# Optimization experiments

Measured on AMD Instinct MI355X. Metric: run time of the kernel, lower is better.

The kernel has to match this reference:

```python
import jax, jax.numpy as jnp
import numpy as np

B, SEQ, DIMS, HEAD, LAYER = 1, 8192, 1024, 16, 4
HD = DIMS // HEAD  # 64
MEL_MAX = 2595.0 * np.log10(1.0 + 4000.0 / 200.0)  # 2595*log10(21)


def _ln(x, g, b, eps=1e-5):
    m = x.mean(-1, keepdims=True)
    v = ((x - m) ** 2).mean(-1, keepdims=True)
    return (x - m) * jax.lax.rsqrt(v + eps) * g + b


def _freq_vec():
    # mask=None branch of _compute_freqs with x=None: 200*scale/1000
    scale = 10.0 ** (jnp.linspace(0.0, MEL_MAX, HD // 2) / 2595.0) - 1.0
    return 200.0 * scale / 1000.0


def _rope(x, mag):
    # x: [b,h,c,hd]; mag: [b,c] = original input mean over feature dim
    c = x.shape[2]
    t = jnp.arange(c, dtype=x.dtype)
    ang = t[:, None] * _freq_vec()[None, :]          # [c, hd/2]
    cosA, sinA = jnp.cos(ang), jnp.sin(ang)
    m = mag[:, None, :, None]                        # [b,1,c,1] (valid: b==1)
    xr, xi = x[..., 0::2], x[..., 1::2]              # complex pairs (x[2i], x[2i+1])
    outr = m * (xr * cosA - xi * sinA)
    outi = m * (xr * sinA + xi * cosA)
    return jnp.stack([outr, outi], axis=-1).reshape(x.shape)


def setup_inputs() -> dict:
    key = jax.random.key(0)
    ks = jax.random.split(key, 4)
    s = 0.02
    return {
        "x": jax.random.normal(ks[0], (B, SEQ, DIMS), jnp.float32),
        "qn_g": jnp.ones((DIMS,), jnp.float32),
        "qn_b": jnp.zeros((DIMS,), jnp.float32),
        "Wq": jax.random.normal(ks[1], (DIMS, DIMS), jnp.float32) * s,
        "bq": jnp.zeros((DIMS,), jnp.float32),
        "kvn_g": jnp.ones((DIMS,), jnp.float32),
        "kvn_b": jnp.zeros((DIMS,), jnp.float32),
        "Wkv": jax.random.normal(ks[2], (DIMS, 2 * DIMS), jnp.float32) * s,
        "bkv": jnp.zeros((2 * DIMS,), jnp.float32),
        "Wout": jax.random.normal(ks[3], (DIMS, DIMS), jnp.float32) * s,
        "bout": jnp.zeros((DIMS,), jnp.float32),
        "ln_g": jnp.ones((HD,), jnp.float32),
        "ln_b": jnp.zeros((HD,), jnp.float32),
        "skip": 0,
    }


def reference(x, qn_g, qn_b, Wq, bq, kvn_g, kvn_b, Wkv, bkv, Wout, bout, ln_g, ln_b, skip):
    b, c, d = x.shape
    # q branch: prenorm -> linear -> [b,h,c,hd]
    q = (_ln(x, qn_g, qn_b) @ Wq + bq).reshape(b, c, HEAD, HD).transpose(0, 2, 1, 3)
    # kv branch: prenorm -> linear -> split (kv, h, d) -> [2,b,h,c,hd]
    kv = (_ln(x, kvn_g, kvn_b) @ Wkv + bkv).reshape(b, c, 2, HEAD, HD).transpose(2, 0, 3, 1, 4)
    k, v = kv[0], kv[1]
    # rotary with magnitude = x.mean(-1) (xa=x passed for both q and k)
    mag = x.mean(-1)  # [b,c]
    q = _rope(q, mag)
    k = _rope(k, mag)
    # strided sparse kv: skip-int path, pattern=None
    stride = max(1, LAYER - int(skip))
    ks_ = k[:, :, ::stride, :]
    vs_ = v[:, :, ::stride, :]
    # per-head LayerNorm on q and strided k, then SDPA (non-causal, mask=None)
    qn = _ln(q, ln_g, ln_b)
    kn = _ln(ks_, ln_g, ln_b)
    scores = jnp.einsum('bhqd,bhkd->bhqk', qn, kn) / np.sqrt(HD).astype(np.float32)
    a = jnp.einsum('bhqk,bhkd->bhqd', jax.nn.softmax(scores, axis=-1), vs_)
    return a.transpose(0, 2, 1, 3).reshape(b, c, d) @ Wout + bout
```

## Files before the change

### kernel.cpp

```cpp
#include <hip/hip_runtime.h>
#include <hip/hip_bf16.h>
#include <math.h>

#define SEQ 8192
#define DIMS 1024
#define NH 16
#define HD 64

typedef _Float16 h16;
typedef __attribute__((ext_vector_type(8))) _Float16 f16x8;
typedef __attribute__((ext_vector_type(4))) _Float16 h16x4;
typedef __attribute__((ext_vector_type(4))) float f32x4;

#if defined(__has_builtin)
#if __has_builtin(__builtin_amdgcn_global_load_lds)
#define USE_GLOAD 1
#endif
#endif
#ifndef USE_GLOAD
#define USE_GLOAD 0
#endif

__device__ __forceinline__ void gload16(h16* lds, const h16* g){
#if USE_GLOAD
  __builtin_amdgcn_global_load_lds((const __attribute__((address_space(1))) void*)g,
                                   (__attribute__((address_space(3))) void*)lds, 16, 0, 0);
#endif
}

__global__ void k_ln_stats(const float* __restrict__ x, h16* __restrict__ xhat,
                           float* __restrict__ mag){
  const int row = blockIdx.x, t = threadIdx.x;
  float4 v = ((const float4*)(x + (size_t)row*DIMS))[t];
  float s = v.x+v.y+v.z+v.w;
  float s2 = v.x*v.x+v.y*v.y+v.z*v.z+v.w*v.w;
  #pragma unroll
  for(int m=1;m<64;m<<=1){ s += __shfl_xor(s,m,64); s2 += __shfl_xor(s2,m,64); }
  __shared__ float ls[4], ls2[4];
  const int wid = t>>6;
  if((t&63)==0){ ls[wid]=s; ls2[wid]=s2; }
  __syncthreads();
  s  = ls[0]+ls[1]+ls[2]+ls[3];
  s2 = ls2[0]+ls2[1]+ls2[2]+ls2[3];
  const float mean = s*(1.f/DIMS);
  const float var  = s2*(1.f/DIMS) - mean*mean;
  const float rstd = rsqrtf(var + 1e-5f);
  if(t==0) mag[row] = mean;
  h16x4 o;
  o[0] = (h16)((v.x-mean)*rstd); o[1] = (h16)((v.y-mean)*rstd);
  o[2] = (h16)((v.z-mean)*rstd); o[3] = (h16)((v.w-mean)*rstd);
  ((h16x4*)(xhat + (size_t)row*DIMS))[t] = o;
}

__global__ void k_freq(double* __restrict__ fr){
  const int d = threadIdx.x;
  if(d < 32) fr[d] = 0.2 * (pow(21.0, (double)d / 31.0) - 1.0);
}

__global__ void k_sincos(const double* __restrict__ fr, float2* __restrict__ tab){
  const int id = blockIdx.x*256 + threadIdx.x;
  const int t = id >> 5, d = id & 31;
  const double ang = (double)t * fr[d];
  const double k = rint(ang * 0.15915494309189535);
  const float red = (float)(ang - k * 6.283185307179586);
  float s, c;
  __sincosf(red, &s, &c);
  tab[id] = make_float2(c, s);
}

__global__ void k_fold_part(const float* __restrict__ W, const float* __restrict__ bln,
                            float* __restrict__ part, const int C){
  const int j = blockIdx.x*256 + threadIdx.x;
  const int ib = blockIdx.y;
  if(j >= C) return;
  float acc = 0.f;
  const int i0 = ib*64;
  #pragma unroll 4
  for(int i=i0;i<i0+64;i++) acc += bln[i]*W[(size_t)i*C + j];
  part[(size_t)ib*C + j] = acc;
}
__global__ void k_fold_sum(const float* __restrict__ part, const float* __restrict__ b0,
                           float* __restrict__ bias_out, const int C){
  const int j = blockIdx.x*256 + threadIdx.x;
  if(j >= C) return;
  float acc = b0[j];
  #pragma unroll
  for(int ib=0; ib<16; ib++) acc += part[(size_t)ib*C + j];
  bias_out[j] = acc;
}

__global__ void k_prep_w(const float* __restrict__ W, const float* __restrict__ g,
                         h16* __restrict__ Wt, const int R, const int C){
  __shared__ float tile[64][65];
  const int c0 = blockIdx.x*64, r0 = blockIdx.y*64;
  const int t = threadIdx.x;
  const int cl = t & 63, rl0 = t >> 6;
  #pragma unroll
  for(int i=0;i<16;i++){
    const int r = rl0 + i*4;
    const float w = W[(size_t)(r0+r)*C + c0 + cl];
    const float gg = g ? g[r0+r] : 1.f;
    tile[r][cl] = w*gg;
  }
  __syncthreads();
  const int jl = t >> 2, ic = (t & 3)*16;
  h16* dst = Wt + (size_t)(c0+jl)*R + r0 + ic;
  #pragma unroll
  for(int i=0;i<16;i+=4){
    h16x4 o;
    o[0] = (h16)tile[ic+i+0][jl];
    o[1] = (h16)tile[ic+i+1][jl];
    o[2] = (h16)tile[ic+i+2][jl];
    o[3] = (h16)tile[ic+i+3][jl];
    *(h16x4*)(dst + i) = o;
  }
}

template<int MODE>
__global__ __launch_bounds__(256) void k_gemm(
    const h16* __restrict__ A, const h16* __restrict__ Bt,
    const float* __restrict__ bias, float* __restrict__ Cf,
    h16* __restrict__ OutB, h16* __restrict__ vT,
    const float* __restrict__ mag, const float2* __restrict__ tab,
    const float* __restrict__ lg, const float* __restrict__ lb,
    const int N, const int* __restrict__ skip_p){
  int M = SEQ, pitchA = DIMS, st = 1;
  if(MODE==2){
    st = max(1, 4 - skip_p[0]);
    M = (SEQ + st - 1)/st;
    pitchA = st*DIMS;
  }
  const int m0 = blockIdx.y*128, n0 = blockIdx.x*128;
  if(m0 >= M) return;
  __shared__ h16 smem[(MODE==2) ? 128*136 : 8192];
  h16* As = smem;
  h16* Bs = smem + 4096;
  const int t = threadIdx.x;
  const int w = t>>6, l = t&63, l4 = l>>4, l16 = l&15;
  const int wm = w>>1, wn = w&1;
  f32x4 acc[4][4];
  #pragma unroll
  for(int i=0;i<4;i++)
    #pragma unroll
    for(int j=0;j<4;j++)
      #pragma unroll
      for(int r=0;r<4;r++) acc[i][j][r] = 0.f;
  for(int k0=0;k0<1024;k0+=32){
    __syncthreads();
    #pragma unroll
    for(int c=t;c<512;c+=256){
      const int row = c>>2, kp = (c&3)*8;
      int ar = m0+row; if(ar > M-1) ar = M-1;
#if USE_GLOAD
      gload16(&As[row*32+kp], A + (size_t)ar*pitchA + k0 + kp);
      gload16(&Bs[row*32+kp], Bt + (size_t)(n0+row)*1024 + k0 + kp);
#else
      *(f16x8*)(&As[row*32+kp]) = *(const f16x8*)(A + (size_t)ar*pitchA + k0 + kp);
      *(f16x8*)(&Bs[row*32+kp]) = *(const f16x8*)(Bt + (size_t)(n0+row)*1024 + k0 + kp);
#endif
    }
    __syncthreads();
    f16x8 af[4], bfr[4];
    #pragma unroll
    for(int i=0;i<4;i++){
      af[i]  = *(const f16x8*)(&As[(wm*64 + i*16 + l16)*32 + l4*8]);
      bfr[i] = *(const f16x8*)(&Bs[(wn*64 + i*16 + l16)*32 + l4*8]);
    }
    #pragma unroll
    for(int i=0;i<4;i++)
      #pragma unroll
      for(int j=0;j<4;j++)
        acc[i][j] = __builtin_amdgcn_mfma_f32_16x16x32_f16(af[i], bfr[j], acc[i][j], 0,0,0);
  }

  if(MODE==0){
    #pragma unroll
    for(int i=0;i<4;i++){
      const int rb = m0 + wm*64 + i*16 + l4*4;
      #pragma unroll
      for(int j=0;j<4;j++){
        const int col = n0 + wn*64 + j*16 + l16;
        const float bb = bias[col];
        #pragma unroll
        for(int r=0;r<4;r++)
          Cf[(size_t)(rb+r)*N + col] = acc[i][j][r] + bb;
      }
    }
    return;
  }

  float biasv[4];
  #pragma unroll
  for(int j=0;j<4;j++) biasv[j] = bias[n0 + wn*64 + j*16 + l16];

  const bool vpath = (MODE==2) && (n0 >= 1024);
  if(!vpath){
    float gv[4], bv[4];
    #pragma unroll
    for(int j=0;j<4;j++){ gv[j] = lg[j*16+l16]; bv[j] = lb[j*16+l16]; }
    const int h = (n0>>6) + wn;
    const float scl = (MODE==1) ? 0.125f*1.44269504f : 1.0f;
    const float sgn = (l16&1) ? 1.f : -1.f;
    #pragma unroll
    for(int i=0;i<4;i++){
      #pragma unroll
      for(int r=0;r<4;r++){
        int row = m0 + wm*64 + i*16 + l4*4 + r;
        const int rowc = (row < M) ? row : (M-1);
        const int tpos = (MODE==2) ? rowc*st : rowc;
        const float mg = mag[tpos];
        float v[4], pr[4], o4[4];
        #pragma unroll
        for(int j=0;j<4;j++) v[j] = acc[i][j][r] + biasv[j];
        #pragma unroll
        for(int j=0;j<4;j++) pr[j] = __shfl_xor(v[j], 1);
        float s1 = 0.f, s2 = 0.f;
        #pragma unroll
        for(int j=0;j<4;j++){
          const float2 cs = tab[(size_t)tpos*32 + j*8 + (l16>>1)];
          const float e = mg * (v[j]*cs.x + sgn*pr[j]*cs.y);
          o4[j] = e; s1 += e; s2 += e*e;
        }
        #pragma unroll
        for(int mm=1;mm<16;mm<<=1){ s1 += __shfl_xor(s1,mm,64); s2 += __shfl_xor(s2,mm,64); }
        const float mean = s1*(1.f/HD);
        const float var  = s2*(1.f/HD) - mean*mean;
        const float rstd = rsqrtf(var + 1e-5f);
        if(row < M){
          h16* dst = OutB + ((size_t)h*SEQ + row)*HD;
          #pragma unroll
          for(int j=0;j<4;j++)
            dst[j*16 + l16] = (h16)(((o4[j]-mean)*rstd*gv[j] + bv[j])*scl);
        }
      }
    }
  } else {
    __syncthreads();
    #pragma unroll
    for(int i=0;i<4;i++)
      #pragma unroll
      for(int j=0;j<4;j++)
        #pragma unroll
        for(int r=0;r<4;r++){
          const int key = wm*64 + i*16 + l4*4 + r;
          smem[(wn*64 + j*16 + l16)*136 + key] = (h16)(acc[i][j][r] + biasv[j]);
        }
    __syncthreads();
    const int rowT = t>>1, dh = rowT & 63, hloc = rowT>>6;
    const int hglob = ((n0-1024)>>6) + hloc;
    const h16* src = &smem[rowT*136 + (t&1)*64];
    h16* dstv = vT + ((size_t)hglob*HD + dh)*SEQ + m0 + (t&1)*64;
    #pragma unroll
    for(int c=0;c<64;c+=4)
      *(h16x4*)(dstv+c) = *(const h16x4*)(src+c);
  }
}

__global__ void k_pad_vt(h16* __restrict__ vT, const int* __restrict__ skip_p){
  const int st = max(1, 4 - skip_p[0]);
  const int n_kv = (SEQ + st - 1)/st;
  const int kb = ((n_kv + 63)/64)*64;
  const int pad = min(kb, SEQ) - n_kv;
  if(pad <= 0) return;
  const int total = NH*HD*pad;
  for(int i = threadIdx.x; i < total; i += 256){
    const int key = n_kv + (i % pad);
    const int hd = i / pad;
    vT[(size_t)hd*SEQ + key] = (h16)0.f;
  }
}

__launch_bounds__(256)
__global__ void k_attn(const h16* __restrict__ qn, const h16* __restrict__ kn,
                       const h16* __restrict__ vT, h16* __restrict__ aout,
                       const int* __restrict__ skip_p){
  const int st = max(1, 4 - skip_p[0]);
  const int n_kv = (SEQ + st - 1)/st;
  const int h = blockIdx.x, q0 = blockIdx.y*128;
  const int w = threadIdx.x >> 6, l = threadIdx.x & 63;
  const int l4 = l >> 4, l16 = l & 15;
  __shared__ __align__(16) h16 Kl[2][64*64];
  __shared__ __align__(16) h16 Vl[2][64*64];
  __shared__ __align__(16) h16 Pl[4][16*64];
  const h16* Qh = qn + (size_t)h*SEQ*HD;
  const h16* Kh = kn + (size_t)h*SEQ*HD;
  const h16* Vh = vT + (size_t)h*HD*SEQ;
  const int srow = l >> 3;
  const int scol = ((l & 7) << 4) ^ (srow << 4);
  const int swz  = (l16 & 7) << 4;

  f16x8 onesv;
  #pragma unroll
  for(int i=0;i<8;i++) onesv[i] = (h16)1.f;

  f16x8 qf[2][2];
  #pragma unroll
  for(int mi=0;mi<2;mi++)
    #pragma unroll
    for(int ks=0;ks<2;ks++)
      qf[mi][ks] = *(const f16x8*)(Qh + (size_t)(q0 + w*32 + mi*16 + l16)*HD + ks*32 + l4*8);
  f32x4 o[2][4], osum[2];
  float mrow[2];
  #pragma unroll
  for(int mi=0;mi<2;mi++){
    mrow[mi] = -1e30f;
    #pragma unroll
    for(int r=0;r<4;r++) osum[mi][r] = 0.f;
    #pragma unroll
    for(int j=0;j<4;j++)
      #pragma unroll
      for(int r=0;r<4;r++) o[mi][j][r] = 0.f;
  }

  const int nkb = (n_kv + 63) >> 6;
  int cur = 0;
  {
    const int r0 = w*16;
    gload16(&Kl[0][(r0+0)*64], (const h16*)((const char*)(Kh + (size_t)(r0+srow)*HD) + scol));
    gload16(&Kl[0][(r0+8)*64], (const h16*)((const char*)(Kh + (size_t)(r0+8+srow)*HD) + scol));
    gload16(&Vl[0][(r0+0)*64], (const h16*)((const char*)(Vh + (size_t)(r0+srow)*SEQ) + scol));
    gload16(&Vl[0][(r0+8)*64], (const h16*)((const char*)(Vh + (size_t)(r0+8+srow)*SEQ) + scol));
  }
  for(int kb=0; kb<nkb; kb++){
    asm volatile("s_waitcnt vmcnt(0)" ::: "memory");
    __syncthreads();
    if(kb+1 < nkb){
      const int kb2 = (kb+1)*64, r0 = w*16, nxt = cur^1;
      gload16(&Kl[nxt][(r0+0)*64], (const h16*)((const char*)(Kh + (size_t)(kb2+r0+srow)*HD) + scol));
      gload16(&Kl[nxt][(r0+8)*64], (const h16*)((const char*)(Kh + (size_t)(kb2+r0+8+srow)*HD) + scol));
      gload16(&Vl[nxt][(r0+0)*64], (const h16*)((const char*)(Vh + (size_t)(r0+srow)*SEQ + kb2) + scol));
      gload16(&Vl[nxt][(r0+8)*64], (const h16*)((const char*)(Vh + (size_t)(r0+8+srow)*SEQ + kb2) + scol));
    }
    f32x4 S[2][4];
    #pragma unroll
    for(int mi=0;mi<2;mi++)
      #pragma unroll
      for(int j=0;j<4;j++)
        #pragma unroll
        for(int r=0;r<4;r++) S[mi][j][r] = 0.f;
    __builtin_amdgcn_s_setprio(1);
    #pragma unroll
    for(int ks=0;ks<2;ks++){
      f16x8 kf[4];
      #pragma unroll
      for(int nj=0;nj<4;nj++)
        kf[nj] = *(const f16x8*)((const char*)&Kl[cur][(nj*16+l16)*64] + ((ks*64 + l4*16) ^ swz));
      #pragma unroll
      for(int mi=0;mi<2;mi++)
        #pragma unroll
        for(int nj=0;nj<4;nj++)
          S[mi][nj] = __builtin_amdgcn_mfma_f32_16x16x32_f16(kf[nj], qf[mi][ks], S[mi][nj], 0,0,0);
    }
    __builtin_amdgcn_s_setprio(0);
    if(kb == nkb-1 && (n_kv & 63)){
      const int kbase = kb*64;
      #pragma unroll
      for(int nj=0;nj<4;nj++){
        const int keyb = kbase + nj*16 + l4*4;
        #pragma unroll
        for(int r=0;r<4;r++)
          if(keyb + r >= n_kv){ S[0][nj][r] = -1e30f; S[1][nj][r] = -1e30f; }
      }
    }
    #pragma unroll
    for(int mi=0;mi<2;mi++){
      f32x4 t4;
      #pragma unroll
      for(int r=0;r<4;r++)
        t4[r] = fmaxf(fmaxf(S[mi][0][r],S[mi][1][r]), fmaxf(S[mi][2][r],S[mi][3][r]));
      float mx = fmaxf(fmaxf(t4[0],t4[1]), fmaxf(t4[2],t4[3]));
      mx = fmaxf(mx, __shfl_xor(mx,16,64));
      mx = fmaxf(mx, __shfl_xor(mx,32,64));
      if(!__all(mx <= mrow[mi] + 11.5f)){
        const float mnew = fmaxf(mrow[mi], mx);
        const float fac = exp2f(mrow[mi] - mnew);
        mrow[mi] = mnew;
        #pragma unroll
        for(int r=0;r<4;r++){
          const float f2 = __shfl(fac, (l & 48) | (l4*4 + r), 64);
          #pragma unroll
          for(int j2=0;j2<4;j2++) o[mi][j2][r] *= f2;
          osum[mi][r] *= f2;
        }
      }
      #pragma unroll
      for(int nj=0;nj<4;nj++){
        #pragma unroll
        for(int r=0;r<4;r++)
          S[mi][nj][r] = exp2f(S[mi][nj][r] - mrow[mi]);
        const unsigned plo = __builtin_bit_cast(unsigned,
            __builtin_amdgcn_cvt_pkrtz(S[mi][nj][0], S[mi][nj][1]));
        const unsigned phi = __builtin_bit_cast(unsigned,
            __builtin_amdgcn_cvt_pkrtz(S[mi][nj][2], S[mi][nj][3]));
        uint2 pw; pw.x = plo; pw.y = phi;
        *(uint2*)((char*)&Pl[w][l16*64] + ((nj*32 + l4*8) ^ swz)) = pw;
      }
      asm volatile("s_waitcnt lgkmcnt(0)" ::: "memory");
      __builtin_amdgcn_sched_barrier(0);
      __builtin_amdgcn_s_setprio(1);
      #pragma unroll
      for(int ks=0;ks<2;ks++){
        const f16x8 pf = *(const f16x8*)((const char*)&Pl[w][l16*64] + ((ks*64 + l4*16) ^ swz));
        #pragma unroll
        for(int j2=0;j2<4;j2++){
          const f16x8 vf = *(const f16x8*)((const char*)&Vl[cur][(j2*16+l16)*64] + ((ks*64 + l4*16) ^ swz));
          o[mi][j2] = __builtin_amdgcn_mfma_f32_16x16x32_f16(pf, vf, o[mi][j2], 0,0,0);
        }
        osum[mi] = __builtin_amdgcn_mfma_f32_16x16x32_f16(pf, onesv, osum[mi], 0,0,0);
      }
      __builtin_amdgcn_s_setprio(0);
    }
    cur ^= 1;
  }
  #pragma unroll
  for(int mi=0;mi<2;mi++){
    #pragma unroll
    for(int r=0;r<4;r++){
      const float iv = 1.f/osum[mi][r];
      const int row = q0 + w*32 + mi*16 + l4*4 + r;
      #pragma unroll
      for(int j2=0;j2<4;j2++)
        aout[(size_t)row*DIMS + h*HD + j2*16 + l16] = (h16)(o[mi][j2][r]*iv);
    }
  }
}

extern "C" void kernel_launch(void* const* d_in, const int* in_sizes, int n_in,
                              void* d_out, int out_size, void* d_ws, size_t ws_size,
                              hipStream_t stream){
  const float* x    = (const float*)d_in[0];
  const float* qn_g = (const float*)d_in[1];
  const float* qn_b = (const float*)d_in[2];
  const float* Wq   = (const float*)d_in[3];
  const float* bq   = (const float*)d_in[4];
  const float* kvn_g= (const float*)d_in[5];
  const float* kvn_b= (const float*)d_in[6];
  const float* Wkv  = (const float*)d_in[7];
  const float* bkv  = (const float*)d_in[8];
  const float* Wout = (const float*)d_in[9];
  const float* bout = (const float*)d_in[10];
  const float* ln_g = (const float*)d_in[11];
  const float* ln_b = (const float*)d_in[12];
  const int*  skip  = (const int*)d_in[13];

  if(ws_size < (size_t)79*1000*1000) return;

  char* p = (char*)d_ws;
  size_t off = 0;
  auto take = [&](size_t n)->char*{
    char* r = p + off; off = (off + n + 255) & ~(size_t)255; return r;
  };
  h16*    xhat = (h16*)   take((size_t)SEQ*DIMS*2);
  float*  mag  = (float*) take((size_t)SEQ*4);
  float2* tab  = (float2*)take((size_t)SEQ*32*8);
  h16*    WqT  = (h16*)   take((size_t)1024*1024*2);
  h16*    WkvT = (h16*)   take((size_t)2048*1024*2);
  h16*    WoutT= (h16*)   take((size_t)1024*1024*2);
  float*  bqp  = (float*) take(1024*4);
  float*  bkvp = (float*) take(2048*4);
  h16*    qn   = (h16*)   take((size_t)NH*SEQ*HD*2);
  h16*    kn   = (h16*)   take((size_t)NH*SEQ*HD*2);
  h16*    vT   = (h16*)   take((size_t)NH*HD*SEQ*2);
  float*  part = (float*) take((size_t)16*2048*4);
  double* freq = (double*)take(32*8);
  h16*    abuf = xhat;

  k_ln_stats<<<dim3(SEQ), dim3(256), 0, stream>>>(x, xhat, mag);
  k_freq<<<dim3(1), dim3(32), 0, stream>>>(freq);
  k_sincos<<<dim3(SEQ*32/256), dim3(256), 0, stream>>>(freq, tab);
  k_fold_part<<<dim3(4,16), dim3(256), 0, stream>>>(Wq, qn_b, part, 1024);
  k_fold_sum<<<dim3(4), dim3(256), 0, stream>>>(part, bq, bqp, 1024);
  k_fold_part<<<dim3(8,16), dim3(256), 0, stream>>>(Wkv, kvn_b, part, 2048);
  k_fold_sum<<<dim3(8), dim3(256), 0, stream>>>(part, bkv, bkvp, 2048);
  k_prep_w<<<dim3(16,16), dim3(256), 0, stream>>>(Wq,  qn_g,  WqT,  1024, 1024);
  k_prep_w<<<dim3(32,16), dim3(256), 0, stream>>>(Wkv, kvn_g, WkvT, 1024, 2048);
  k_prep_w<<<dim3(16,16), dim3(256), 0, stream>>>(Wout, nullptr, WoutT, 1024, 1024);
  k_gemm<1><<<dim3(8,64),  dim3(256), 0, stream>>>(xhat, WqT,  bqp, nullptr, qn, nullptr,
                                                   mag, tab, ln_g, ln_b, 1024, skip);
  k_gemm<2><<<dim3(16,64), dim3(256), 0, stream>>>(xhat, WkvT, bkvp, nullptr, kn, vT,
                                                   mag, tab, ln_g, ln_b, 2048, skip);
  k_pad_vt<<<dim3(1), dim3(256), 0, stream>>>(vT, skip);
  k_attn<<<dim3(16,64), dim3(256), 0, stream>>>(qn, kn, vT, abuf, skip);
  k_gemm<0><<<dim3(8,64), dim3(256), 0, stream>>>(abuf, WoutT, bout, (float*)d_out,
                                                  nullptr, nullptr, nullptr, nullptr,
                                                  nullptr, nullptr, 1024, skip);
}
```

Measured before the change: 297.9 us.

## Single-buffer K/V tiles in attention and use hardware exp2 builtin

```diff
diff --git a/kernel.cpp b/kernel.cpp
--- a/kernel.cpp
+++ b/kernel.cpp
@@ -16,9 +16,15 @@
 #if __has_builtin(__builtin_amdgcn_global_load_lds)
 #define USE_GLOAD 1
 #endif
+#if __has_builtin(__builtin_amdgcn_exp2f)
+#define FEXP2(x) __builtin_amdgcn_exp2f(x)
+#endif
 #endif
 #ifndef USE_GLOAD
 #define USE_GLOAD 0
+#endif
+#ifndef FEXP2
+#define FEXP2(x) exp2f(x)
 #endif
 
 __device__ __forceinline__ void gload16(h16* lds, const h16* g){
@@ -279,8 +285,8 @@
   const int h = blockIdx.x, q0 = blockIdx.y*128;
   const int w = threadIdx.x >> 6, l = threadIdx.x & 63;
   const int l4 = l >> 4, l16 = l & 15;
-  __shared__ __align__(16) h16 Kl[2][64*64];
-  __shared__ __align__(16) h16 Vl[2][64*64];
+  __shared__ __align__(16) h16 Kl[64*64];
+  __shared__ __align__(16) h16 Vl[64*64];
   __shared__ __align__(16) h16 Pl[4][16*64];
   const h16* Qh = qn + (size_t)h*SEQ*HD;
   const h16* Kh = kn + (size_t)h*SEQ*HD;
@@ -292,6 +298,7 @@
   f16x8 onesv;
   #pragma unroll
   for(int i=0;i<8;i++) onesv[i] = (h16)1.f;
+  const f32x4 zf = {0.f, 0.f, 0.f, 0.f};
 
   f16x8 qf[2][2];
   #pragma unroll
@@ -313,50 +320,43 @@
   }
 
   const int nkb = (n_kv + 63) >> 6;
-  int cur = 0;
-  {
-    const int r0 = w*16;
-    gload16(&Kl[0][(r0+0)*64], (const h16*)((const char*)(Kh + (size_t)(r0+srow)*HD) + scol));
-    gload16(&Kl[0][(r0+8)*64], (const h16*)((const char*)(Kh + (size_t)(r0+8+srow)*HD) + scol));
-    gload16(&Vl[0][(r0+0)*64], (const h16*)((const char*)(Vh + (size_t)(r0+srow)*SEQ) + scol));
-    gload16(&Vl[0][(r0+8)*64], (const h16*)((const char*)(Vh + (size_t)(r0+8+srow)*SEQ) + scol));
-  }
   for(int kb=0; kb<nkb; kb++){
-    asm volatile("s_waitcnt vmcnt(0)" ::: "memory");
-    __syncthreads();
-    if(kb+1 < nkb){
-      const int kb2 = (kb+1)*64, r0 = w*16, nxt = cur^1;
-      gload16(&Kl[nxt][(r0+0)*64], (const h16*)((const char*)(Kh + (size_t)(kb2+r0+srow)*HD) + scol));
-      gload16(&Kl[nxt][(r0+8)*64], (const h16*)((const char*)(Kh + (size_t)(kb2+r0+8+srow)*HD) + scol));
-      gload16(&Vl[nxt][(r0+0)*64], (const h16*)((const char*)(Vh + (size_t)(r0+srow)*SEQ + kb2) + scol));
-      gload16(&Vl[nxt][(r0+8)*64], (const h16*)((const char*)(Vh + (size_t)(r0+8+srow)*SEQ + kb2) + scol));
-    }
+    const int kb0 = kb*64, r0 = w*16;
+    __syncthreads();
+    gload16(&Kl[(r0+0)*64], (const h16*)((const char*)(Kh + (size_t)(kb0+r0+srow)*HD) + scol));
+    gload16(&Kl[(r0+8)*64], (const h16*)((const char*)(Kh + (size_t)(kb0+r0+8+srow)*HD) + scol));
+    gload16(&Vl[(r0+0)*64], (const h16*)((const char*)(Vh + (size_t)(r0+srow)*SEQ + kb0) + scol));
+    gload16(&Vl[(r0+8)*64], (const h16*)((const char*)(Vh + (size_t)(r0+8+srow)*SEQ + kb0) + scol));
+    __syncthreads();
     f32x4 S[2][4];
-    #pragma unroll
-    for(int mi=0;mi<2;mi++)
-      #pragma unroll
-      for(int j=0;j<4;j++)
-        #pragma unroll
-        for(int r=0;r<4;r++) S[mi][j][r] = 0.f;
     __builtin_amdgcn_s_setprio(1);
-    #pragma unroll
-    for(int ks=0;ks<2;ks++){
+    {
       f16x8 kf[4];
       #pragma unroll
       for(int nj=0;nj<4;nj++)
-        kf[nj] = *(const f16x8*)((const char*)&Kl[cur][(nj*16+l16)*64] + ((ks*64 + l4*16) ^ swz));
+        kf[nj] = *(const f16x8*)((const char*)&Kl[(nj*16+l16)*64] + ((0*64 + l4*16) ^ swz));
       #pragma unroll
       for(int mi=0;mi<2;mi++)
         #pragma unroll
         for(int nj=0;nj<4;nj++)
-          S[mi][nj] = __builtin_amdgcn_mfma_f32_16x16x32_f16(kf[nj], qf[mi][ks], S[mi][nj], 0,0,0);
+          S[mi][nj] = __builtin_amdgcn_mfma_f32_16x16x32_f16(kf[nj], qf[mi][0], zf, 0,0,0);
+    }
+    {
+      f16x8 kf[4];
+      #pragma unroll
+      for(int nj=0;nj<4;nj++)
+        kf[nj] = *(const f16x8*)((const char*)&Kl[(nj*16+l16)*64] + ((1*64 + l4*16) ^ swz));
+      #pragma unroll
+      for(int mi=0;mi<2;mi++)
+        #pragma unroll
+        for(int nj=0;nj<4;nj++)
+          S[mi][nj] = __builtin_amdgcn_mfma_f32_16x16x32_f16(kf[nj], qf[mi][1], S[mi][nj], 0,0,0);
     }
     __builtin_amdgcn_s_setprio(0);
     if(kb == nkb-1 && (n_kv & 63)){
-      const int kbase = kb*64;
       #pragma unroll
       for(int nj=0;nj<4;nj++){
-        const int keyb = kbase + nj*16 + l4*4;
+        const int keyb = kb0 + nj*16 + l4*4;
         #pragma unroll
         for(int r=0;r<4;r++)
           if(keyb + r >= n_kv){ S[0][nj][r] = -1e30f; S[1][nj][r] = -1e30f; }
@@ -373,7 +373,7 @@
       mx = fmaxf(mx, __shfl_xor(mx,32,64));
       if(!__all(mx <= mrow[mi] + 11.5f)){
         const float mnew = fmaxf(mrow[mi], mx);
-        const float fac = exp2f(mrow[mi] - mnew);
+        const float fac = FEXP2(mrow[mi] - mnew);
         mrow[mi] = mnew;
         #pragma unroll
         for(int r=0;r<4;r++){
@@ -387,7 +387,7 @@
       for(int nj=0;nj<4;nj++){
         #pragma unroll
         for(int r=0;r<4;r++)
-          S[mi][nj][r] = exp2f(S[mi][nj][r] - mrow[mi]);
+          S[mi][nj][r] = FEXP2(S[mi][nj][r] - mrow[mi]);
         const unsigned plo = __builtin_bit_cast(unsigned,
             __builtin_amdgcn_cvt_pkrtz(S[mi][nj][0], S[mi][nj][1]));
         const unsigned phi = __builtin_bit_cast(unsigned,
@@ -403,14 +403,13 @@
         const f16x8 pf = *(const f16x8*)((const char*)&Pl[w][l16*64] + ((ks*64 + l4*16) ^ swz));
         #pragma unroll
         for(int j2=0;j2<4;j2++){
-          const f16x8 vf = *(const f16x8*)((const char*)&Vl[cur][(j2*16+l16)*64] + ((ks*64 + l4*16) ^ swz));
+          const f16x8 vf = *(const f16x8*)((const char*)&Vl[(j2*16+l16)*64] + ((ks*64 + l4*16) ^ swz));
           o[mi][j2] = __builtin_amdgcn_mfma_f32_16x16x32_f16(pf, vf, o[mi][j2], 0,0,0);
         }
         osum[mi] = __builtin_amdgcn_mfma_f32_16x16x32_f16(pf, onesv, osum[mi], 0,0,0);
       }
       __builtin_amdgcn_s_setprio(0);
     }
-    cur ^= 1;
   }
   #pragma unroll
   for(int mi=0;mi<2;mi++){
```

Measured after the change: 267.3 us. 10.3% less time.
